# Kernel tuning notes

Hardware: AMD Instinct MI355X
Metric: run time of the kernel (lower is better)

Reference implementation:

```python
import jax, jax.numpy as jnp
import numpy as np

ALPHA = 0.2  # LeakyReLU negative slope
N, F_IN, F_OUT = 8192, 512, 64
NEG_INF = -9e15


def setup_inputs() -> dict:
    key = jax.random.key(0)
    k1, k2, k3, k4 = jax.random.split(key, 4)
    inp = jax.random.normal(k1, (N, F_IN), dtype=jnp.float32)
    adj = jax.random.randint(k2, (N, N), 0, 2, dtype=jnp.int32)
    W = jax.random.normal(k3, (F_IN, F_OUT), dtype=jnp.float32) * (1.414 / np.sqrt(F_IN))
    a = jax.random.normal(k4, (2 * F_OUT, 1), dtype=jnp.float32) * 0.1
    return {"input": inp, "adj": adj, "W": W, "a": a, "sparse": 0}


def reference(input, adj, W, a, sparse):
    h = input @ W  # [N, F_out]
    # Decompose concat([h_i, h_j]) @ a into additive src/dst terms (same math,
    # avoids the O(N^2 * 2F) intermediate): e_ij = leakyrelu(h_i@a1 + h_j@a2)
    f_src = h @ a[:F_OUT]   # [N, 1]
    f_dst = h @ a[F_OUT:]   # [N, 1]
    e = jax.nn.leaky_relu(f_src + f_dst.T, ALPHA)  # [N, N]
    attention = jnp.where(adj > 0, e, NEG_INF)
    attention = jax.nn.softmax(attention, axis=1)
    h_prime = attention @ h  # [N, F_out]
    return jax.nn.leaky_relu(h_prime, 0.01)[None]  # concat=True path; default F.leaky_relu slope 0.01
```

## Files before the change

kernel.cpp:

```cpp
#include <hip/hip_runtime.h>
#include <hip/hip_bf16.h>

#define N 8192
#define FIN 512
#define FOUT 64
#define ALPHA 0.2f

typedef __bf16 bf16x8 __attribute__((ext_vector_type(8)));
typedef __bf16 bf16x4 __attribute__((ext_vector_type(4)));
typedef float f32x4 __attribute__((ext_vector_type(4)));
typedef int i32x4 __attribute__((ext_vector_type(4)));


__device__ __forceinline__ unsigned enc_f(float x) {
    unsigned u = __float_as_uint(x);
    return (u & 0x80000000u) ? ~u : (u | 0x80000000u);
}
__device__ __forceinline__ float dec_f(unsigned u) {
    return (u & 0x80000000u) ? __uint_as_float(u & 0x7FFFFFFFu) : __uint_as_float(~u);
}

__device__ __forceinline__ void glds16(const void* g, void* l) {
    __builtin_amdgcn_global_load_lds((const __attribute__((address_space(1))) void*)g,
                                     (__attribute__((address_space(3))) void*)l, 16, 0, 0);
}
#define SFENCE() __builtin_amdgcn_sched_barrier(0)

__global__ __launch_bounds__(64) void k_wt(const float* __restrict__ W,
                                           __bf16* __restrict__ WtG) {
    const int g = blockIdx.x * 64 + threadIdx.x;
    const int k = g >> 3;
    const int f0 = (g & 7) * 8;
    const float4 w0 = *(const float4*)(W + (size_t)k * FOUT + f0);
    const float4 w1 = *(const float4*)(W + (size_t)k * FOUT + f0 + 4);
    WtG[(size_t)(f0 + 0) * FIN + k] = (__bf16)w0.x;
    WtG[(size_t)(f0 + 1) * FIN + k] = (__bf16)w0.y;
    WtG[(size_t)(f0 + 2) * FIN + k] = (__bf16)w0.z;
    WtG[(size_t)(f0 + 3) * FIN + k] = (__bf16)w0.w;
    WtG[(size_t)(f0 + 4) * FIN + k] = (__bf16)w1.x;
    WtG[(size_t)(f0 + 5) * FIN + k] = (__bf16)w1.y;
    WtG[(size_t)(f0 + 6) * FIN + k] = (__bf16)w1.z;
    WtG[(size_t)(f0 + 7) * FIN + k] = (__bf16)w1.w;
}

__global__ __launch_bounds__(64) void k12(const float* __restrict__ in,
                                          const __bf16* __restrict__ WtG,
                                          const float* __restrict__ a,
                                          float* __restrict__ f_src,
                                          float* __restrict__ f_dst,
                                          unsigned* __restrict__ Mkey,
                                          __bf16* __restrict__ hT) {
    __shared__ __bf16 tb[64][16];
    const int lane = threadIdx.x;
    const int m = lane & 15, quad = lane >> 4;
    const int i0 = blockIdx.x * 16;

    f32x4 acc[4];
#pragma unroll
    for (int t = 0; t < 4; ++t) acc[t] = (f32x4){0.f, 0.f, 0.f, 0.f};

    const float* arow = in + (size_t)(i0 + m) * FIN + quad * 8;
    for (int k0 = 0; k0 < FIN; k0 += 32) {
        const float4 x0 = *(const float4*)(arow + k0);
        const float4 x1 = *(const float4*)(arow + k0 + 4);
        bf16x8 af;
        af[0] = (__bf16)x0.x; af[1] = (__bf16)x0.y; af[2] = (__bf16)x0.z; af[3] = (__bf16)x0.w;
        af[4] = (__bf16)x1.x; af[5] = (__bf16)x1.y; af[6] = (__bf16)x1.z; af[7] = (__bf16)x1.w;
#pragma unroll
        for (int t = 0; t < 4; ++t) {
            const bf16x8 bf = *(const bf16x8*)(WtG + (size_t)(t * 16 + m) * FIN + k0 + quad * 8);
            acc[t] = __builtin_amdgcn_mfma_f32_16x16x32_bf16(af, bf, acc[t], 0, 0, 0);
        }
    }
    float s1[4], s2[4];
#pragma unroll
    for (int r = 0; r < 4; ++r) { s1[r] = 0.f; s2[r] = 0.f; }
#pragma unroll
    for (int t = 0; t < 4; ++t) {
        const float a1 = a[t * 16 + m], a2 = a[64 + t * 16 + m];
#pragma unroll
        for (int r = 0; r < 4; ++r) {
            s1[r] += acc[t][r] * a1;
            s2[r] += acc[t][r] * a2;
        }
    }
#pragma unroll
    for (int off = 1; off <= 8; off <<= 1)
#pragma unroll
        for (int r = 0; r < 4; ++r) {
            s1[r] += __shfl_xor(s1[r], off);
            s2[r] += __shfl_xor(s2[r], off);
        }
    float lm = -1e30f;
    if (m == 0) {
#pragma unroll
        for (int r = 0; r < 4; ++r) {
            f_src[i0 + quad * 4 + r] = s1[r];
            f_dst[i0 + quad * 4 + r] = s2[r];
            lm = fmaxf(lm, s2[r]);
        }
    }
    lm = fmaxf(lm, __shfl_xor(lm, 16));
    lm = fmaxf(lm, __shfl_xor(lm, 32));
    if (lane == 0) atomicMax(Mkey, enc_f(lm));

#pragma unroll
    for (int t = 0; t < 4; ++t)
#pragma unroll
        for (int r = 0; r < 4; ++r) tb[t * 16 + m][quad * 4 + r] = (__bf16)acc[t][r];
    __syncthreads();
    {
        const int f = lane;
        const bf16x8 v0 = *(const bf16x8*)&tb[f][0];
        const bf16x8 v1 = *(const bf16x8*)&tb[f][8];
        *(bf16x8*)(hT + (size_t)f * N + i0) = v0;
        *(bf16x8*)(hT + (size_t)f * N + i0 + 8) = v1;
    }
}

constexpr int JT = 128;

__global__ __launch_bounds__(256, 3) void k3_attn(const int* __restrict__ adj,
                                                  const float* __restrict__ f_src,
                                                  const float* __restrict__ fdstG,
                                                  const unsigned* __restrict__ Mkey,
                                                  const __bf16* __restrict__ hT,
                                                  float* __restrict__ num_part,
                                                  float* __restrict__ lsum_part) {
    __shared__ __bf16 sh[2][64][JT];
    __shared__ __bf16 wl[4][16][JT];
    __shared__ float sfd[1024];
    const int tid = threadIdx.x;
    const int wv = tid >> 6, lane = tid & 63;
    const int m = lane & 15, quad = lane >> 4;
    const int rpar = lane >> 5;
    const int col4 = (lane & 31) * 4;
    const int i0 = blockIdx.x * 64 + wv * 16;
    const int jb = blockIdx.y * 1024;
    const float LOG2E = 1.44269504088896f;

    *(f32x4*)&sfd[tid * 4] = *(const f32x4*)(fdstG + jb + tid * 4);
    const float M = dec_f(*Mkey);
    float fsr[16], shl[16];
#pragma unroll
    for (int r = 0; r < 16; ++r) {
        const float fs =
            __uint_as_float(__builtin_amdgcn_readfirstlane(__float_as_uint(f_src[i0 + r])));
        const float t0 = fs + M;
        fsr[r] = fs;
        shl[r] = fmaxf(t0, ALPHA * t0) * LOG2E;
    }
    const __bf16* gsrc[4];
#pragma unroll
    for (int i = 0; i < 4; ++i) {
        const int f = (wv * 4 + i) * 4 + (lane >> 4);
        const int csw = ((lane & 15) * 8) ^ ((f & 7) << 3);
        gsrc[i] = hT + (size_t)f * N + jb + csw;
    }
    const int* apL = adj + (size_t)(i0 + rpar) * N + jb + col4;

    SFENCE();
    __syncthreads();
    SFENCE();

    f32x4 acc[4];
#pragma unroll
    for (int t = 0; t < 4; ++t) acc[t] = (f32x4){0.f, 0.f, 0.f, 0.f};
    f32x4 accl = (f32x4){0.f, 0.f, 0.f, 0.f};
    bf16x8 bones;
#pragma unroll
    for (int jj = 0; jj < 8; ++jj) bones[jj] = (__bf16)(m == 0 ? 1.0f : 0.0f);

    i32x4 adjv[2][8];
#pragma unroll
    for (int i = 0; i < 4; ++i) glds16(gsrc[i], &sh[0][(wv * 4 + i) * 4][0]);
    SFENCE();
#pragma unroll
    for (int v = 0; v < 8; ++v)
        adjv[0][v] = __builtin_nontemporal_load((const i32x4*)(apL + (size_t)(2 * v) * N));
    SFENCE();

#pragma unroll
    for (int t = 0; t < 8; ++t) {
        const int jt = t * JT;
        const int cur = t & 1, nxt = cur ^ 1;
        asm volatile("s_waitcnt vmcnt(8)" ::: "memory");
        SFENCE();
        __builtin_amdgcn_s_barrier();
        SFENCE();
        if (t < 7) {
#pragma unroll
            for (int i = 0; i < 4; ++i)
                glds16(gsrc[i] + jt + JT, &sh[nxt][(wv * 4 + i) * 4][0]);
        }
        SFENCE();
        if (t < 7) {
#pragma unroll
            for (int v = 0; v < 8; ++v)
                adjv[nxt][v] = __builtin_nontemporal_load(
                    (const i32x4*)(apL + (size_t)(2 * v) * N + jt + JT));
        }
        SFENCE();
        const f32x4 fd0 = *(const f32x4*)&sfd[jt + col4];
#pragma unroll
        for (int v = 0; v < 8; ++v) {
            const float fs_l = rpar ? fsr[2 * v + 1] : fsr[2 * v];
            const float sh_l = rpar ? shl[2 * v + 1] : shl[2 * v];
            bf16x4 wb;
#pragma unroll
            for (int c = 0; c < 4; ++c) {
                float e = fs_l + fd0[c];
                e = fmaxf(e, ALPHA * e);
                const float ex = __builtin_amdgcn_exp2f(e * LOG2E - sh_l);
                wb[c] = (__bf16)(adjv[cur][v][c] > 0 ? ex : 0.f);
            }
            const int rr = 2 * v + rpar;
            *(bf16x4*)&wl[wv][rr][col4 ^ ((rr & 7) << 3)] = wb;
        }
        SFENCE();
#pragma unroll
        for (int jj0 = 0; jj0 < JT; jj0 += 64) {
#pragma unroll
            for (int u = 0; u < 2; ++u) {
                const int cb = jj0 + u * 32 + quad * 8;
                const int cs = cb ^ ((m & 7) << 3);
                const bf16x8 af = *(const bf16x8*)&wl[wv][m][cs];
#pragma unroll
                for (int tt = 0; tt < 4; ++tt) {
                    const bf16x8 bfr = *(const bf16x8*)&sh[cur][tt * 16 + m][cs];
                    acc[tt] = __builtin_amdgcn_mfma_f32_16x16x32_bf16(af, bfr, acc[tt], 0, 0, 0);
                }
                accl = __builtin_amdgcn_mfma_f32_16x16x32_bf16(af, bones, accl, 0, 0, 0);
            }
        }
        SFENCE();
        if (t < 7) {
            asm volatile("s_waitcnt lgkmcnt(0)" ::: "memory");
            SFENCE();
            __builtin_amdgcn_s_barrier();
            SFENCE();
        }
    }
    float* npb = num_part + (size_t)blockIdx.y * N * FOUT;
#pragma unroll
    for (int t = 0; t < 4; ++t)
#pragma unroll
        for (int r = 0; r < 4; ++r)
            npb[(size_t)(i0 + quad * 4 + r) * FOUT + t * 16 + m] = acc[t][r];
    if (m == 0) {
#pragma unroll
        for (int r = 0; r < 4; ++r)
            lsum_part[(size_t)blockIdx.y * N + i0 + quad * 4 + r] = accl[r];
    }
}

__global__ __launch_bounds__(256) void k4_norm(float* __restrict__ out,
                                               const float* __restrict__ num_part,
                                               const float* __restrict__ lsum_part) {
    const int idx = blockIdx.x * 256 + threadIdx.x;
    const int i = idx >> 6;
    float s = 0.f, l = 0.f;
#pragma unroll
    for (int p = 0; p < 8; ++p) {
        s += num_part[(size_t)p * N * FOUT + idx];
        l += lsum_part[(size_t)p * N + i];
    }
    const float v = s / (l > 0.f ? l : 1.f);
    out[idx] = v > 0.f ? v : 0.01f * v;
}

extern "C" void kernel_launch(void* const* d_in, const int* in_sizes, int n_in,
                              void* d_out, int out_size, void* d_ws, size_t ws_size,
                              hipStream_t stream) {
    const float* in = (const float*)d_in[0];
    const int* adj = (const int*)d_in[1];
    const float* W = (const float*)d_in[2];
    const float* a = (const float*)d_in[3];
    float* out = (float*)d_out;

    char* ws = (char*)d_ws;
    unsigned* Mkey = (unsigned*)ws;
    float* f_src = (float*)(ws + 32832);
    float* f_dst = (float*)(ws + 65600);
    __bf16* WtG = (__bf16*)(ws + 98368);
    __bf16* hT = (__bf16*)(ws + 163904);
    float* num_part = (float*)(ws + 1212480);
    float* lsum_part = (float*)(ws + 17989696);

    hipMemsetAsync(ws, 0, 64, stream);

    k_wt<<<64, 64, 0, stream>>>(W, WtG);
    k12<<<N / 16, 64, 0, stream>>>(in, WtG, a, f_src, f_dst, Mkey, hT);

    dim3 g3(N / 64, 8);
    k3_attn<<<g3, 256, 0, stream>>>(adj, f_src, f_dst, Mkey, hT, num_part, lsum_part);
    k4_norm<<<(N * FOUT) / 256, 256, 0, stream>>>(out, num_part, lsum_part);
}
```

Baseline: 390.2 us.

## Single-buffer hT tile, prefetch adjacency two tiles ahead, raise occupancy

The attention kernel now keeps one LDS buffer for the hT tile instead of two, and prefetches the adjacency rows two tiles ahead in registers. It loads the next hT tile only after a barrier once the current tile has been consumed. Launch bounds rise from 3 to 4 blocks per CU, helped by the smaller LDS footprint, and per-lane f_src values replace the readfirstlane arrays. The Mkey memset is folded into the k_wt kernel to save a launch. The cost is an extra barrier per tile and exposed hT load latency, traded for more resident waves and deeper prefetch of the adjacency stream.

```diff
diff --git a/kernel.cpp b/kernel.cpp
--- a/kernel.cpp
+++ b/kernel.cpp
@@ -27,7 +27,9 @@
 #define SFENCE() __builtin_amdgcn_sched_barrier(0)
 
 __global__ __launch_bounds__(64) void k_wt(const float* __restrict__ W,
-                                           __bf16* __restrict__ WtG) {
+                                           __bf16* __restrict__ WtG,
+                                           unsigned* __restrict__ Mkey) {
+    if (blockIdx.x == 0 && threadIdx.x == 0) *Mkey = 0u;
     const int g = blockIdx.x * 64 + threadIdx.x;
     const int k = g >> 3;
     const int f0 = (g & 7) * 8;
@@ -119,15 +121,16 @@
 }
 
 constexpr int JT = 128;
-
-__global__ __launch_bounds__(256, 3) void k3_attn(const int* __restrict__ adj,
+constexpr int NT = 1024 / JT;
+
+__global__ __launch_bounds__(256, 4) void k3_attn(const int* __restrict__ adj,
                                                   const float* __restrict__ f_src,
                                                   const float* __restrict__ fdstG,
                                                   const unsigned* __restrict__ Mkey,
                                                   const __bf16* __restrict__ hT,
                                                   float* __restrict__ num_part,
                                                   float* __restrict__ lsum_part) {
-    __shared__ __bf16 sh[2][64][JT];
+    __shared__ __bf16 sh[64][JT];
     __shared__ __bf16 wl[4][16][JT];
     __shared__ float sfd[1024];
     const int tid = threadIdx.x;
@@ -141,14 +144,13 @@
 
     *(f32x4*)&sfd[tid * 4] = *(const f32x4*)(fdstG + jb + tid * 4);
     const float M = dec_f(*Mkey);
-    float fsr[16], shl[16];
-#pragma unroll
-    for (int r = 0; r < 16; ++r) {
-        const float fs =
-            __uint_as_float(__builtin_amdgcn_readfirstlane(__float_as_uint(f_src[i0 + r])));
+    float fsv[8], shv[8];
+#pragma unroll
+    for (int v = 0; v < 8; ++v) {
+        const float fs = f_src[i0 + 2 * v + rpar];
         const float t0 = fs + M;
-        fsr[r] = fs;
-        shl[r] = fmaxf(t0, ALPHA * t0) * LOG2E;
+        fsv[v] = fs;
+        shv[v] = fmaxf(t0, ALPHA * t0) * LOG2E;
     }
     const __bf16* gsrc[4];
 #pragma unroll
@@ -159,10 +161,6 @@
     }
     const int* apL = adj + (size_t)(i0 + rpar) * N + jb + col4;
 
-    SFENCE();
-    __syncthreads();
-    SFENCE();
-
     f32x4 acc[4];
 #pragma unroll
     for (int t = 0; t < 4; ++t) acc[t] = (f32x4){0.f, 0.f, 0.f, 0.f};
@@ -173,45 +171,35 @@
 
     i32x4 adjv[2][8];
 #pragma unroll
-    for (int i = 0; i < 4; ++i) glds16(gsrc[i], &sh[0][(wv * 4 + i) * 4][0]);
+    for (int i = 0; i < 4; ++i) glds16(gsrc[i], &sh[(wv * 4 + i) * 4][0]);
     SFENCE();
 #pragma unroll
     for (int v = 0; v < 8; ++v)
         adjv[0][v] = __builtin_nontemporal_load((const i32x4*)(apL + (size_t)(2 * v) * N));
     SFENCE();
-
-#pragma unroll
-    for (int t = 0; t < 8; ++t) {
+#pragma unroll
+    for (int v = 0; v < 8; ++v)
+        adjv[1][v] = __builtin_nontemporal_load((const i32x4*)(apL + (size_t)(2 * v) * N + JT));
+    SFENCE();
+    asm volatile("s_waitcnt lgkmcnt(0)" ::: "memory");
+    asm volatile("s_waitcnt vmcnt(16)" ::: "memory");
+    SFENCE();
+    __builtin_amdgcn_s_barrier();
+    SFENCE();
+
+#pragma unroll
+    for (int t = 0; t < NT; ++t) {
         const int jt = t * JT;
-        const int cur = t & 1, nxt = cur ^ 1;
-        asm volatile("s_waitcnt vmcnt(8)" ::: "memory");
-        SFENCE();
-        __builtin_amdgcn_s_barrier();
-        SFENCE();
-        if (t < 7) {
-#pragma unroll
-            for (int i = 0; i < 4; ++i)
-                glds16(gsrc[i] + jt + JT, &sh[nxt][(wv * 4 + i) * 4][0]);
-        }
-        SFENCE();
-        if (t < 7) {
-#pragma unroll
-            for (int v = 0; v < 8; ++v)
-                adjv[nxt][v] = __builtin_nontemporal_load(
-                    (const i32x4*)(apL + (size_t)(2 * v) * N + jt + JT));
-        }
-        SFENCE();
-        const f32x4 fd0 = *(const f32x4*)&sfd[jt + col4];
+        const int cur = t & 1;
+        const f32x4 fd = *(const f32x4*)&sfd[jt + col4];
 #pragma unroll
         for (int v = 0; v < 8; ++v) {
-            const float fs_l = rpar ? fsr[2 * v + 1] : fsr[2 * v];
-            const float sh_l = rpar ? shl[2 * v + 1] : shl[2 * v];
             bf16x4 wb;
 #pragma unroll
             for (int c = 0; c < 4; ++c) {
-                float e = fs_l + fd0[c];
+                float e = fsv[v] + fd[c];
                 e = fmaxf(e, ALPHA * e);
-                const float ex = __builtin_amdgcn_exp2f(e * LOG2E - sh_l);
+                const float ex = __builtin_amdgcn_exp2f(e * LOG2E - shv[v]);
                 wb[c] = (__bf16)(adjv[cur][v][c] > 0 ? ex : 0.f);
             }
             const int rr = 2 * v + rpar;
@@ -227,15 +215,32 @@
                 const bf16x8 af = *(const bf16x8*)&wl[wv][m][cs];
 #pragma unroll
                 for (int tt = 0; tt < 4; ++tt) {
-                    const bf16x8 bfr = *(const bf16x8*)&sh[cur][tt * 16 + m][cs];
+                    const bf16x8 bfr = *(const bf16x8*)&sh[tt * 16 + m][cs];
                     acc[tt] = __builtin_amdgcn_mfma_f32_16x16x32_bf16(af, bfr, acc[tt], 0, 0, 0);
                 }
                 accl = __builtin_amdgcn_mfma_f32_16x16x32_bf16(af, bones, accl, 0, 0, 0);
             }
         }
         SFENCE();
-        if (t < 7) {
+        if (t < NT - 1) {
             asm volatile("s_waitcnt lgkmcnt(0)" ::: "memory");
+            SFENCE();
+            __builtin_amdgcn_s_barrier();
+            SFENCE();
+#pragma unroll
+            for (int i = 0; i < 4; ++i)
+                glds16(gsrc[i] + jt + JT, &sh[(wv * 4 + i) * 4][0]);
+            SFENCE();
+            if (t < NT - 2) {
+#pragma unroll
+                for (int v = 0; v < 8; ++v)
+                    adjv[cur][v] = __builtin_nontemporal_load(
+                        (const i32x4*)(apL + (size_t)(2 * v) * N + jt + 2 * JT));
+                SFENCE();
+                asm volatile("s_waitcnt vmcnt(8)" ::: "memory");
+            } else {
+                asm volatile("s_waitcnt vmcnt(0)" ::: "memory");
+            }
             SFENCE();
             __builtin_amdgcn_s_barrier();
             SFENCE();
@@ -287,9 +292,7 @@
     float* num_part = (float*)(ws + 1212480);
     float* lsum_part = (float*)(ws + 17989696);
 
-    hipMemsetAsync(ws, 0, 64, stream);
-
-    k_wt<<<64, 64, 0, stream>>>(W, WtG);
+    k_wt<<<64, 64, 0, stream>>>(W, WtG, Mkey);
     k12<<<N / 16, 64, 0, stream>>>(in, WtG, a, f_src, f_dst, Mkey, hT);
 
     dim3 g3(N / 64, 8);
```

New measurement: 436.0 us. 11.7% more time.

## Split k12 projection K-loop across four waves and fold Mkey reset into k_wt

Applied to the files above, without the earlier changes.

The projection kernel now runs 256 threads per block, and each wave computes a quarter of the K=512 reduction. Partial MFMA accumulators are summed through shared memory, and the attention-vector dot products are reduced across waves before the max atomic. This gives more memory-level parallelism per 16-row block in the input-read-bound projection, at the cost of extra LDS traffic and barriers. Separately, the hipMemsetAsync that cleared Mkey is removed and the reset is done inside k_wt, saving one launch.

```diff
diff --git a/kernel.cpp b/kernel.cpp
--- a/kernel.cpp
+++ b/kernel.cpp
@@ -27,7 +27,9 @@
 #define SFENCE() __builtin_amdgcn_sched_barrier(0)
 
 __global__ __launch_bounds__(64) void k_wt(const float* __restrict__ W,
-                                           __bf16* __restrict__ WtG) {
+                                           __bf16* __restrict__ WtG,
+                                           unsigned* __restrict__ Mkey) {
+    if (blockIdx.x == 0 && threadIdx.x == 0) *Mkey = 0u;
     const int g = blockIdx.x * 64 + threadIdx.x;
     const int k = g >> 3;
     const int f0 = (g & 7) * 8;
@@ -43,15 +45,18 @@
     WtG[(size_t)(f0 + 7) * FIN + k] = (__bf16)w1.w;
 }
 
-__global__ __launch_bounds__(64) void k12(const float* __restrict__ in,
-                                          const __bf16* __restrict__ WtG,
-                                          const float* __restrict__ a,
-                                          float* __restrict__ f_src,
-                                          float* __restrict__ f_dst,
-                                          unsigned* __restrict__ Mkey,
-                                          __bf16* __restrict__ hT) {
+__global__ __launch_bounds__(256) void k12(const float* __restrict__ in,
+                                           const __bf16* __restrict__ WtG,
+                                           const float* __restrict__ a,
+                                           float* __restrict__ f_src,
+                                           float* __restrict__ f_dst,
+                                           unsigned* __restrict__ Mkey,
+                                           __bf16* __restrict__ hT) {
+    __shared__ float red[4][4][4][64];
+    __shared__ float sred[4][4][4][2];
     __shared__ __bf16 tb[64][16];
-    const int lane = threadIdx.x;
+    const int tid = threadIdx.x;
+    const int wv = tid >> 6, lane = tid & 63;
     const int m = lane & 15, quad = lane >> 4;
     const int i0 = blockIdx.x * 16;
 
@@ -59,8 +64,10 @@
 #pragma unroll
     for (int t = 0; t < 4; ++t) acc[t] = (f32x4){0.f, 0.f, 0.f, 0.f};
 
-    const float* arow = in + (size_t)(i0 + m) * FIN + quad * 8;
-    for (int k0 = 0; k0 < FIN; k0 += 32) {
+    const float* arow = in + (size_t)(i0 + m) * FIN + wv * 128 + quad * 8;
+    const __bf16* wrow = WtG + wv * 128 + quad * 8;
+#pragma unroll
+    for (int k0 = 0; k0 < 128; k0 += 32) {
         const float4 x0 = *(const float4*)(arow + k0);
         const float4 x1 = *(const float4*)(arow + k0 + 4);
         bf16x8 af;
@@ -68,48 +75,56 @@
         af[4] = (__bf16)x1.x; af[5] = (__bf16)x1.y; af[6] = (__bf16)x1.z; af[7] = (__bf16)x1.w;
 #pragma unroll
         for (int t = 0; t < 4; ++t) {
-            const bf16x8 bf = *(const bf16x8*)(WtG + (size_t)(t * 16 + m) * FIN + k0 + quad * 8);
+            const bf16x8 bf = *(const bf16x8*)(wrow + (size_t)(t * 16 + m) * FIN + k0);
             acc[t] = __builtin_amdgcn_mfma_f32_16x16x32_bf16(af, bf, acc[t], 0, 0, 0);
         }
     }
-    float s1[4], s2[4];
-#pragma unroll
-    for (int r = 0; r < 4; ++r) { s1[r] = 0.f; s2[r] = 0.f; }
-#pragma unroll
-    for (int t = 0; t < 4; ++t) {
-        const float a1 = a[t * 16 + m], a2 = a[64 + t * 16 + m];
+#pragma unroll
+    for (int t = 0; t < 4; ++t)
+#pragma unroll
+        for (int r = 0; r < 4; ++r) red[wv][t][r][lane] = acc[t][r];
+    __syncthreads();
+    float facc[4];
+#pragma unroll
+    for (int r = 0; r < 4; ++r)
+        facc[r] = red[0][wv][r][lane] + red[1][wv][r][lane] +
+                  red[2][wv][r][lane] + red[3][wv][r][lane];
+    const float a1 = a[wv * 16 + m], a2 = a[64 + wv * 16 + m];
+    float p1[4], p2[4];
+#pragma unroll
+    for (int r = 0; r < 4; ++r) { p1[r] = facc[r] * a1; p2[r] = facc[r] * a2; }
+#pragma unroll
+    for (int off = 1; off <= 8; off <<= 1)
 #pragma unroll
         for (int r = 0; r < 4; ++r) {
-            s1[r] += acc[t][r] * a1;
-            s2[r] += acc[t][r] * a2;
-        }
-    }
-#pragma unroll
-    for (int off = 1; off <= 8; off <<= 1)
+            p1[r] += __shfl_xor(p1[r], off);
+            p2[r] += __shfl_xor(p2[r], off);
+        }
+    if (m == 0)
 #pragma unroll
         for (int r = 0; r < 4; ++r) {
-            s1[r] += __shfl_xor(s1[r], off);
-            s2[r] += __shfl_xor(s2[r], off);
-        }
-    float lm = -1e30f;
-    if (m == 0) {
-#pragma unroll
-        for (int r = 0; r < 4; ++r) {
-            f_src[i0 + quad * 4 + r] = s1[r];
-            f_dst[i0 + quad * 4 + r] = s2[r];
-            lm = fmaxf(lm, s2[r]);
-        }
-    }
-    lm = fmaxf(lm, __shfl_xor(lm, 16));
-    lm = fmaxf(lm, __shfl_xor(lm, 32));
-    if (lane == 0) atomicMax(Mkey, enc_f(lm));
-
-#pragma unroll
-    for (int t = 0; t < 4; ++t)
-#pragma unroll
-        for (int r = 0; r < 4; ++r) tb[t * 16 + m][quad * 4 + r] = (__bf16)acc[t][r];
+            sred[wv][quad][r][0] = p1[r];
+            sred[wv][quad][r][1] = p2[r];
+        }
+#pragma unroll
+    for (int r = 0; r < 4; ++r) tb[wv * 16 + m][quad * 4 + r] = (__bf16)facc[r];
     __syncthreads();
-    {
+    if (wv == 0) {
+        float lm = -1e30f;
+        if (lane < 16) {
+            const int q = lane >> 2, r = lane & 3;
+            const float s1 = sred[0][q][r][0] + sred[1][q][r][0] +
+                             sred[2][q][r][0] + sred[3][q][r][0];
+            const float s2 = sred[0][q][r][1] + sred[1][q][r][1] +
+                             sred[2][q][r][1] + sred[3][q][r][1];
+            f_src[i0 + lane] = s1;
+            f_dst[i0 + lane] = s2;
+            lm = s2;
+        }
+#pragma unroll
+        for (int off = 1; off <= 32; off <<= 1) lm = fmaxf(lm, __shfl_xor(lm, off));
+        if (lane == 0) atomicMax(Mkey, enc_f(lm));
+    } else if (wv == 1) {
         const int f = lane;
         const bf16x8 v0 = *(const bf16x8*)&tb[f][0];
         const bf16x8 v1 = *(const bf16x8*)&tb[f][8];
@@ -287,10 +302,8 @@
     float* num_part = (float*)(ws + 1212480);
     float* lsum_part = (float*)(ws + 17989696);
 
-    hipMemsetAsync(ws, 0, 64, stream);
-
-    k_wt<<<64, 64, 0, stream>>>(W, WtG);
-    k12<<<N / 16, 64, 0, stream>>>(in, WtG, a, f_src, f_dst, Mkey, hT);
+    k_wt<<<64, 64, 0, stream>>>(W, WtG, Mkey);
+    k12<<<N / 16, 256, 0, stream>>>(in, WtG, a, f_src, f_dst, Mkey, hT);
 
     dim3 g3(N / 64, 8);
     k3_attn<<<g3, 256, 0, stream>>>(adj, f_src, f_dst, Mkey, hT, num_part, lsum_part);
```

After: 387.2 us. No clear change (-0.8%).
